# Optimization experiments

Hardware: AMD Instinct MI355X
Metric: run time of the kernel (lower is better)

## Reference

```python
import jax, jax.numpy as jnp
import numpy as np

COMMITMENT_COST = 0.25
N_EMBED = 1024
EMB_DIM = 256

def setup_inputs() -> dict:
    key = jax.random.key(0)
    k1, k2 = jax.random.split(key)
    z = jax.random.normal(k1, (32, EMB_DIM, 32, 32), dtype=jnp.float32)
    # embedding.weight.data.uniform_(-1/n_embed, 1/n_embed)
    embedding = jax.random.uniform(k2, (N_EMBED, EMB_DIM), dtype=jnp.float32,
                                   minval=-1.0 / N_EMBED, maxval=1.0 / N_EMBED)
    return {"z": z, "embedding": embedding}

def reference(z, embedding):
    # NCHW -> NHWC
    zp = jnp.transpose(z, (0, 2, 3, 1))            # [B,H,W,D]
    in_shape = zp.shape
    flat = zp.reshape(-1, in_shape[-1])            # [N,D]
    # squared L2 distances (argmin equivalent to p=2 cdist argmin)
    d2 = (jnp.sum(flat * flat, axis=1, keepdims=True)
          - 2.0 * (flat @ embedding.T)
          + jnp.sum(embedding * embedding, axis=1))  # [N,K]
    idx = jnp.argmin(d2, axis=1)                   # [N]
    # one-hot @ codebook == direct gather
    z_quant = embedding[idx].reshape(in_shape)     # [B,H,W,D]
    codebook_loss = jnp.mean((z_quant - jax.lax.stop_gradient(zp)) ** 2)
    commitment_loss = jnp.mean((zp - jax.lax.stop_gradient(z_quant)) ** 2)
    loss = codebook_loss + COMMITMENT_COST * commitment_loss
    # straight-through estimator
    z_st = zp + jax.lax.stop_gradient(z_quant - zp)
    z_st = jnp.transpose(z_st, (0, 3, 1, 2))       # NHWC -> NCHW
    return (z_st, loss, codebook_loss, commitment_loss)
```

## Files before the change

### kernel.cpp

```cpp
#include <hip/hip_runtime.h>
#include <hip/hip_bf16.h>
#include <stdint.h>


typedef short v8s __attribute__((ext_vector_type(8)));
typedef float v4f __attribute__((ext_vector_type(4)));

__device__ inline unsigned short f2bf(float f) {
    uint32_t u = __float_as_uint(f);
    return (unsigned short)((u + 0x7fffu + ((u >> 16) & 1u)) >> 16);
}

__global__ __launch_bounds__(512) void k_prep_a(const float* __restrict__ z,
                                                unsigned short* __restrict__ Abf) {
    int tid = threadIdx.x;
    int b = blockIdx.x >> 4, hw0 = (blockIdx.x & 15) << 6;
    int t15 = tid & 15, dblk = tid >> 4;
    const float* zp = z + ((size_t)b << 18) + (size_t)(dblk << 3) * 1024 + hw0 + (t15 << 2);
    float4 L[8];
#pragma unroll
    for (int j = 0; j < 8; j++)
        L[j] = *(const float4*)(zp + (size_t)j * 1024);
    const float* Lf = (const float*)L;
    v8s* Aout = (v8s*)Abf + ((size_t)(b * 1024 + hw0 + (t15 << 2))) * 32 + dblk;
#pragma unroll
    for (int c = 0; c < 4; c++) {
        union { v8s v; unsigned short s[8]; } u;
#pragma unroll
        for (int j = 0; j < 8; j++) u.s[j] = f2bf(Lf[j * 4 + c]);
        Aout[(size_t)c * 32] = u.v;
    }
}

__global__ __launch_bounds__(256) void k_prep_e(const float* __restrict__ E,
                                                v8s* __restrict__ Esw,
                                                float* __restrict__ nE,
                                                float* __restrict__ accum) {
    __shared__ float Ef[16][264];
    int q = blockIdx.x, tid = threadIdx.x;
    const float4* Ein = (const float4*)(E + ((size_t)q << 12));
#pragma unroll
    for (int i = 0; i < 4; i++) {
        int f4 = i * 256 + tid;
        int row = f4 >> 6, c4 = (f4 & 63) << 2;
        *(float4*)&Ef[row][c4] = Ein[f4];
    }
    __syncthreads();
    {
        int c = tid >> 4, l = tid & 15;
        float s = 0.f;
#pragma unroll
        for (int j = 0; j < 16; j++) { float v = Ef[c][l + 16 * j]; s += v * v; }
#pragma unroll
        for (int off = 1; off < 16; off <<= 1) s += __shfl_xor(s, off);
        if (l == 0) nE[q * 16 + c] = 0.5f * s;
    }
#pragma unroll
    for (int i = 0; i < 2; i++) {
        int u = tid + i * 256;
        int um = u & 15, ug = (u >> 4) & 3, udc = (u >> 6) & 7;
        int d0 = udc * 32 + ug * 8;
        union { v8s v; unsigned short s[8]; } pk;
#pragma unroll
        for (int e = 0; e < 8; e++) pk.s[e] = f2bf(Ef[um][d0 + e]);
        Esw[((size_t)q << 9) + u] = pk.v;
    }
    if (q == 0 && tid == 0) accum[0] = 0.f;
}

__global__ __launch_bounds__(256) void k_main(
        const unsigned short* __restrict__ Abf,
        const v8s* __restrict__ Esw,
        const float* __restrict__ nE,
        const float* __restrict__ z,
        const float* __restrict__ E,
        float* __restrict__ out,
        float* __restrict__ accum) {
    __shared__ union {
        v8s   B[2][2048];
        float Eg[32 * 260];
    } S;
    __shared__ float nEl[1024];
    __shared__ int   idxLds[128];
    __shared__ float w4[4];

    int tid = threadIdx.x;
    int lane = tid & 63, w = tid >> 6;
    int g = lane >> 4, m = lane & 15;
    int R0 = blockIdx.x << 7;
    int b = R0 >> 10, hw0 = R0 & 1023;

#pragma unroll
    for (int i = 0; i < 4; i++) nEl[tid + i * 256] = nE[tid + i * 256];

    v8s a[2][8];
    {
        const v8s* Ap = (const v8s*)Abf;
#pragma unroll
        for (int s = 0; s < 2; s++) {
            int row = R0 + w * 32 + s * 16 + m;
#pragma unroll
            for (int dc = 0; dc < 8; dc++)
                a[s][dc] = Ap[(size_t)row * 32 + dc * 4 + g];
        }
    }

#define STAGE(ch, buf)                                                        \
    {                                                                         \
        _Pragma("unroll")                                                     \
        for (int j = 0; j < 8; j++) {                                         \
            __builtin_amdgcn_global_load_lds(                                 \
                (const __attribute__((address_space(1))) void*)               \
                    (Esw + ((size_t)(ch) << 11) + (j << 8) + tid),            \
                (__attribute__((address_space(3))) void*)                     \
                    &S.B[buf][(j << 8) + (w << 6)],                           \
                16, 0, 0);                                                    \
        }                                                                     \
    }

    float best[2][4]; int bidx[2][4];
#pragma unroll
    for (int s = 0; s < 2; s++)
#pragma unroll
        for (int r = 0; r < 4; r++) { best[s][r] = 3.4e38f; bidx[s][r] = 0; }

    STAGE(0, 0);
#pragma unroll 1
    for (int ct = 0; ct < 16; ct++) {
        int cur = ct & 1;
        __syncthreads();
        if (ct < 15) STAGE(ct + 1, cur ^ 1);
        float ne[4];
#pragma unroll
        for (int t = 0; t < 4; t++) ne[t] = nEl[(ct << 6) + t * 16 + m];
        v4f acc[4][2];
#pragma unroll
        for (int t = 0; t < 4; t++)
#pragma unroll
            for (int s = 0; s < 2; s++) acc[t][s] = (v4f){0.f, 0.f, 0.f, 0.f};
#pragma unroll
        for (int dc = 0; dc < 8; dc++) {
#pragma unroll
            for (int t = 0; t < 4; t++) {
                v8s bf = S.B[cur][t * 512 + dc * 64 + g * 16 + m];
                acc[t][0] = __builtin_amdgcn_mfma_f32_16x16x32_bf16(a[0][dc], bf, acc[t][0], 0, 0, 0);
                acc[t][1] = __builtin_amdgcn_mfma_f32_16x16x32_bf16(a[1][dc], bf, acc[t][1], 0, 0, 0);
            }
        }
#pragma unroll
        for (int t = 0; t < 4; t++) {
            int code = (ct << 6) + t * 16 + m;
#pragma unroll
            for (int r = 0; r < 4; r++) {
                float s0 = ne[t] - acc[t][0][r];
                if (s0 < best[0][r]) { best[0][r] = s0; bidx[0][r] = code; }
                float s1 = ne[t] - acc[t][1][r];
                if (s1 < best[1][r]) { best[1][r] = s1; bidx[1][r] = code; }
            }
        }
    }

#pragma unroll
    for (int s = 0; s < 2; s++)
#pragma unroll
        for (int r = 0; r < 4; r++) {
            uint32_t sb = __float_as_uint(best[s][r]);
            sb = (sb & 0x80000000u) ? ~sb : (sb | 0x80000000u);
            unsigned long long pk = ((unsigned long long)sb << 32) | (uint32_t)bidx[s][r];
#pragma unroll
            for (int off = 1; off < 16; off <<= 1) {
                unsigned long long o = __shfl_xor(pk, off);
                if (o < pk) pk = o;
            }
            if (m == 0)
                idxLds[w * 32 + s * 16 + g * 4 + r] = (int)(pk & 0xffffffffu);
        }

    float lsum = 0.f;
    const float* zb = z + ((size_t)b << 18);
    float* ob = out + ((size_t)b << 18);
    int jj = (tid & 7) << 2, dt = tid >> 3;
#pragma unroll 1
    for (int h = 0; h < 4; h++) {
        __syncthreads();
#pragma unroll
        for (int i = 0; i < 8; i++) {
            int row = w + (i << 2);
            int k = idxLds[(h << 5) + row];
            float4 v = ((const float4*)(E + ((size_t)k << 8)))[lane];
            *(float4*)&S.Eg[row * 260 + (lane << 2)] = v;
        }
        __syncthreads();
#pragma unroll
        for (int i = 0; i < 8; i++) {
            int d = dt + (i << 5);
            size_t o = (size_t)d * 1024 + hw0 + (h << 5) + jj;
            float4 zv = *(const float4*)(zb + o);
            float4 ev;
            ev.x = S.Eg[(jj + 0) * 260 + d]; ev.y = S.Eg[(jj + 1) * 260 + d];
            ev.z = S.Eg[(jj + 2) * 260 + d]; ev.w = S.Eg[(jj + 3) * 260 + d];
            *(float4*)(ob + o) = ev;
            float dx = ev.x - zv.x, dy = ev.y - zv.y;
            float dz2 = ev.z - zv.z, dw = ev.w - zv.w;
            lsum += dx * dx + dy * dy + dz2 * dz2 + dw * dw;
        }
    }
#pragma unroll
    for (int off = 1; off < 64; off <<= 1) lsum += __shfl_xor(lsum, off);
    if ((tid & 63) == 0) w4[w] = lsum;
    __syncthreads();
    if (tid == 0) atomicAdd(accum, w4[0] + w4[1] + w4[2] + w4[3]);
#undef STAGE
}

__global__ void k_loss(const float* __restrict__ accum, float* __restrict__ out) {
    if (threadIdx.x == 0) {
        float s = accum[0] * (1.0f / 8388608.0f);
        out[8388608] = 1.25f * s;
        out[8388609] = s;
        out[8388610] = s;
    }
}

extern "C" void kernel_launch(void* const* d_in, const int* in_sizes, int n_in,
                              void* d_out, int out_size, void* d_ws, size_t ws_size,
                              hipStream_t stream) {
    const float* z = (const float*)d_in[0];
    const float* E = (const float*)d_in[1];
    char* ws = (char*)d_ws;
    unsigned short* Abf   = (unsigned short*)(ws);
    v8s*            Esw   = (v8s*)(ws + 16777216);
    float*          nE    = (float*)(ws + 17301504);
    float*          accum = (float*)(ws + 17305600);
    float* out = (float*)d_out;

    hipLaunchKernelGGL(k_prep_e, dim3(64),  dim3(256), 0, stream, E, Esw, nE, accum);
    hipLaunchKernelGGL(k_prep_a, dim3(512), dim3(512), 0, stream, z, Abf);
    hipLaunchKernelGGL(k_main,   dim3(256), dim3(256), 0, stream,
                       Abf, Esw, nE, z, E, out, accum);
    hipLaunchKernelGGL(k_loss,   dim3(1),   dim3(64),  0, stream, accum, out);
}
```

Before: 131.1 us.

## Double waves per block in main kernel and swizzle gather epilogue layout

The main VQ kernel now runs 512 threads per block, with each wave owning 16 rows instead of 32. This halves per-wave MFMA work and register pressure and aims to raise latency hiding, while codebook staging is shared across more waves. The epilogue replaces the padded float LDS tile with an XOR-swizzled float4 layout and uses scalar coalesced stores per channel. The trade-off is more waves contending at each barrier and less B-tile reuse per wave.

```diff
diff --git a/kernel.cpp b/kernel.cpp
--- a/kernel.cpp
+++ b/kernel.cpp
@@ -68,7 +68,7 @@
     if (q == 0 && tid == 0) accum[0] = 0.f;
 }
 
-__global__ __launch_bounds__(256) void k_main(
+__global__ __launch_bounds__(512) void k_main(
         const unsigned short* __restrict__ Abf,
         const v8s* __restrict__ Esw,
         const float* __restrict__ nE,
@@ -77,52 +77,47 @@
         float* __restrict__ out,
         float* __restrict__ accum) {
     __shared__ union {
-        v8s   B[2][2048];
-        float Eg[32 * 260];
+        v8s    B[2][2048];
+        float4 Eg4[2048];
     } S;
     __shared__ float nEl[1024];
     __shared__ int   idxLds[128];
-    __shared__ float w4[4];
+    __shared__ float w8[8];
 
     int tid = threadIdx.x;
     int lane = tid & 63, w = tid >> 6;
     int g = lane >> 4, m = lane & 15;
     int R0 = blockIdx.x << 7;
-    int b = R0 >> 10, hw0 = R0 & 1023;
-
-#pragma unroll
-    for (int i = 0; i < 4; i++) nEl[tid + i * 256] = nE[tid + i * 256];
-
-    v8s a[2][8];
+    int b = R0 >> 10;
+
+#pragma unroll
+    for (int i = 0; i < 2; i++) nEl[tid + i * 512] = nE[tid + i * 512];
+
+    v8s a[8];
     {
         const v8s* Ap = (const v8s*)Abf;
-#pragma unroll
-        for (int s = 0; s < 2; s++) {
-            int row = R0 + w * 32 + s * 16 + m;
-#pragma unroll
-            for (int dc = 0; dc < 8; dc++)
-                a[s][dc] = Ap[(size_t)row * 32 + dc * 4 + g];
-        }
+        int row = R0 + w * 16 + m;
+#pragma unroll
+        for (int dc = 0; dc < 8; dc++)
+            a[dc] = Ap[(size_t)row * 32 + dc * 4 + g];
     }
 
 #define STAGE(ch, buf)                                                        \
     {                                                                         \
         _Pragma("unroll")                                                     \
-        for (int j = 0; j < 8; j++) {                                         \
+        for (int j = 0; j < 4; j++) {                                         \
             __builtin_amdgcn_global_load_lds(                                 \
                 (const __attribute__((address_space(1))) void*)               \
-                    (Esw + ((size_t)(ch) << 11) + (j << 8) + tid),            \
+                    (Esw + ((size_t)(ch) << 11) + (j << 9) + (w << 6) + lane),\
                 (__attribute__((address_space(3))) void*)                     \
-                    &S.B[buf][(j << 8) + (w << 6)],                           \
+                    &S.B[buf][(j << 9) + (w << 6)],                           \
                 16, 0, 0);                                                    \
         }                                                                     \
     }
 
-    float best[2][4]; int bidx[2][4];
-#pragma unroll
-    for (int s = 0; s < 2; s++)
-#pragma unroll
-        for (int r = 0; r < 4; r++) { best[s][r] = 3.4e38f; bidx[s][r] = 0; }
+    float best[4]; int bidx[4];
+#pragma unroll
+    for (int r = 0; r < 4; r++) { best[r] = 3.4e38f; bidx[r] = 0; }
 
     STAGE(0, 0);
 #pragma unroll 1
@@ -133,18 +128,15 @@
         float ne[4];
 #pragma unroll
         for (int t = 0; t < 4; t++) ne[t] = nEl[(ct << 6) + t * 16 + m];
-        v4f acc[4][2];
-#pragma unroll
-        for (int t = 0; t < 4; t++)
-#pragma unroll
-            for (int s = 0; s < 2; s++) acc[t][s] = (v4f){0.f, 0.f, 0.f, 0.f};
+        v4f acc[4];
+#pragma unroll
+        for (int t = 0; t < 4; t++) acc[t] = (v4f){0.f, 0.f, 0.f, 0.f};
 #pragma unroll
         for (int dc = 0; dc < 8; dc++) {
 #pragma unroll
             for (int t = 0; t < 4; t++) {
                 v8s bf = S.B[cur][t * 512 + dc * 64 + g * 16 + m];
-                acc[t][0] = __builtin_amdgcn_mfma_f32_16x16x32_bf16(a[0][dc], bf, acc[t][0], 0, 0, 0);
-                acc[t][1] = __builtin_amdgcn_mfma_f32_16x16x32_bf16(a[1][dc], bf, acc[t][1], 0, 0, 0);
+                acc[t] = __builtin_amdgcn_mfma_f32_16x16x32_bf16(a[dc], bf, acc[t], 0, 0, 0);
             }
         }
 #pragma unroll
@@ -152,64 +144,64 @@
             int code = (ct << 6) + t * 16 + m;
 #pragma unroll
             for (int r = 0; r < 4; r++) {
-                float s0 = ne[t] - acc[t][0][r];
-                if (s0 < best[0][r]) { best[0][r] = s0; bidx[0][r] = code; }
-                float s1 = ne[t] - acc[t][1][r];
-                if (s1 < best[1][r]) { best[1][r] = s1; bidx[1][r] = code; }
+                float s0 = ne[t] - acc[t][r];
+                if (s0 < best[r]) { best[r] = s0; bidx[r] = code; }
             }
         }
     }
 
 #pragma unroll
-    for (int s = 0; s < 2; s++)
-#pragma unroll
-        for (int r = 0; r < 4; r++) {
-            uint32_t sb = __float_as_uint(best[s][r]);
-            sb = (sb & 0x80000000u) ? ~sb : (sb | 0x80000000u);
-            unsigned long long pk = ((unsigned long long)sb << 32) | (uint32_t)bidx[s][r];
-#pragma unroll
-            for (int off = 1; off < 16; off <<= 1) {
-                unsigned long long o = __shfl_xor(pk, off);
-                if (o < pk) pk = o;
-            }
-            if (m == 0)
-                idxLds[w * 32 + s * 16 + g * 4 + r] = (int)(pk & 0xffffffffu);
-        }
+    for (int r = 0; r < 4; r++) {
+        uint32_t sb = __float_as_uint(best[r]);
+        sb = (sb & 0x80000000u) ? ~sb : (sb | 0x80000000u);
+        unsigned long long pk = ((unsigned long long)sb << 32) | (uint32_t)bidx[r];
+#pragma unroll
+        for (int off = 1; off < 16; off <<= 1) {
+            unsigned long long o = __shfl_xor(pk, off);
+            if (o < pk) pk = o;
+        }
+        if (m == 0)
+            idxLds[w * 16 + g * 4 + r] = (int)(pk & 0xffffffffu);
+    }
+    __syncthreads();
 
     float lsum = 0.f;
     const float* zb = z + ((size_t)b << 18);
     float* ob = out + ((size_t)b << 18);
-    int jj = (tid & 7) << 2, dt = tid >> 3;
+    int hwl = tid & 31, dq0 = tid >> 5;
 #pragma unroll 1
-    for (int h = 0; h < 4; h++) {
+    for (int ph = 0; ph < 4; ph++) {
+#pragma unroll
+        for (int i = 0; i < 4; i++) {
+            int row = w + (i << 3);
+            int k = idxLds[(ph << 5) + row];
+            float4 v = ((const float4*)(E + ((size_t)k << 8)))[lane];
+            S.Eg4[(row << 6) + (lane ^ row)] = v;
+        }
         __syncthreads();
-#pragma unroll
-        for (int i = 0; i < 8; i++) {
-            int row = w + (i << 2);
-            int k = idxLds[(h << 5) + row];
-            float4 v = ((const float4*)(E + ((size_t)k << 8)))[lane];
-            *(float4*)&S.Eg[row * 260 + (lane << 2)] = v;
+        int hwp = (R0 & 1023) + (ph << 5) + hwl;
+#pragma unroll
+        for (int i = 0; i < 4; i++) {
+            int dq = dq0 + (i << 4);
+            float4 ev = S.Eg4[(hwl << 6) + (dq ^ hwl)];
+            size_t o = ((size_t)dq << 12) + hwp;
+            float z0 = zb[o], z1 = zb[o + 1024], z2 = zb[o + 2048], z3 = zb[o + 3072];
+            ob[o] = ev.x; ob[o + 1024] = ev.y; ob[o + 2048] = ev.z; ob[o + 3072] = ev.w;
+            float dx = ev.x - z0, dy = ev.y - z1, dz2 = ev.z - z2, dw = ev.w - z3;
+            lsum += dx * dx + dy * dy + dz2 * dz2 + dw * dw;
         }
         __syncthreads();
-#pragma unroll
-        for (int i = 0; i < 8; i++) {
-            int d = dt + (i << 5);
-            size_t o = (size_t)d * 1024 + hw0 + (h << 5) + jj;
-            float4 zv = *(const float4*)(zb + o);
-            float4 ev;
-            ev.x = S.Eg[(jj + 0) * 260 + d]; ev.y = S.Eg[(jj + 1) * 260 + d];
-            ev.z = S.Eg[(jj + 2) * 260 + d]; ev.w = S.Eg[(jj + 3) * 260 + d];
-            *(float4*)(ob + o) = ev;
-            float dx = ev.x - zv.x, dy = ev.y - zv.y;
-            float dz2 = ev.z - zv.z, dw = ev.w - zv.w;
-            lsum += dx * dx + dy * dy + dz2 * dz2 + dw * dw;
-        }
     }
 #pragma unroll
     for (int off = 1; off < 64; off <<= 1) lsum += __shfl_xor(lsum, off);
-    if ((tid & 63) == 0) w4[w] = lsum;
+    if (lane == 0) w8[w] = lsum;
     __syncthreads();
-    if (tid == 0) atomicAdd(accum, w4[0] + w4[1] + w4[2] + w4[3]);
+    if (tid == 0) {
+        float s = 0.f;
+#pragma unroll
+        for (int i = 0; i < 8; i++) s += w8[i];
+        atomicAdd(accum, s);
+    }
 #undef STAGE
 }
 
@@ -236,7 +228,7 @@
 
     hipLaunchKernelGGL(k_prep_e, dim3(64),  dim3(256), 0, stream, E, Esw, nE, accum);
     hipLaunchKernelGGL(k_prep_a, dim3(512), dim3(512), 0, stream, z, Abf);
-    hipLaunchKernelGGL(k_main,   dim3(256), dim3(256), 0, stream,
+    hipLaunchKernelGGL(k_main,   dim3(256), dim3(512), 0, stream,
                        Abf, Esw, nE, z, E, out, accum);
     hipLaunchKernelGGL(k_loss,   dim3(1),   dim3(64),  0, stream, accum, out);
 }
```

New measurement: 127.9 us. 2.5% less time.
